# Optimization experiments

Measured on AMD Instinct MI355X. Metric: run time of the kernel, lower is better.

The kernel has to match this reference:

```python
import jax, jax.numpy as jnp
import numpy as np

WS = 6          # window size
NUM_HEADS = 6
HEAD_DIM = 32   # dim=192 / 6 heads
SCALE = HEAD_DIM ** -0.5


def _rel_pos_index(ws):
    # Faithful to the torch buffer construction (torch.meshgrid default 'ij').
    coords = np.stack(np.meshgrid(np.arange(ws), np.arange(ws), np.arange(ws), indexing='ij'))  # [3,ws,ws,ws]
    flat = coords.reshape(3, -1)                       # [3, ws^3]
    rel = flat[:, :, None] - flat[:, None, :]          # [3, N, N]
    rel = rel.transpose(1, 2, 0).astype(np.int64)      # [N, N, 3]
    rel += ws - 1
    rel[..., 0] *= 3 * ws - 1
    rel[..., 1] *= 2 * ws - 1
    return rel.sum(-1)                                 # [N, N]

REL_INDEX = jnp.asarray(_rel_pos_index(WS))            # [216, 216] int


def setup_inputs() -> dict:
    key = jax.random.key(0)
    k1, k2, k3, k4 = jax.random.split(key, 4)
    B, N, C = 1024, WS ** 3, NUM_HEADS * HEAD_DIM
    return {
        "x": jax.random.normal(k1, (B, N, C), dtype=jnp.float32),
        "qkv_w": jax.random.normal(k2, (3 * C, C), dtype=jnp.float32) * 0.02,
        "proj_w": jax.random.normal(k3, (C, C), dtype=jnp.float32) * 0.02,
        "proj_b": jnp.zeros((C,), dtype=jnp.float32),
        "bias_table": jax.random.normal(k4, ((2 * WS - 1) ** 3, NUM_HEADS), dtype=jnp.float32) * 0.02,
    }


def reference(x, qkv_w, proj_w, proj_b, bias_table):
    B, N, C = x.shape
    H, D = NUM_HEADS, HEAD_DIM
    qkv = jnp.einsum('bnc,fc->bnf', x, qkv_w)              # [B,N,3C]
    qkv = qkv.reshape(B, N, 3, H, D).transpose(2, 0, 3, 1, 4)  # [3,B,H,N,D]
    q, k, v = qkv[0], qkv[1], qkv[2]
    attn = jnp.einsum('bhnd,bhmd->bhnm', q * SCALE, k)     # [B,H,N,N]
    bias = bias_table[REL_INDEX]                           # [N,N,H]
    attn = attn + bias.transpose(2, 0, 1)[None]            # add [1,H,N,N]
    attn = jax.nn.softmax(attn, axis=-1)
    out = jnp.einsum('bhnm,bhmd->bhnd', attn, v)           # [B,H,N,D]
    out = out.transpose(0, 2, 1, 3).reshape(B, N, C)
    return jnp.einsum('bnc,oc->bno', out, proj_w) + proj_b
```

## Files before the change

kernel.cpp:

```cpp
#include <hip/hip_runtime.h>
#include <cstdint>
#include <cstddef>


typedef __attribute__((ext_vector_type(8))) short short8;
typedef __attribute__((ext_vector_type(4))) float f32x4;
typedef unsigned short u16;
typedef unsigned int   u32;

#define SCALE_F 0.17677669529663687f

#define QS_OFF   0
#define KS_OFF   17920
#define VT_OFF   35840
#define PCH_OFF  50688
#define ATTN_LDS 68608

#define PROJ_LDS 76800

__device__ __forceinline__ u16 f2bf(float f) {
  union { float f; u32 u; } v; v.f = f;
  return (u16)((v.u + 0x7fffu + ((v.u >> 16) & 1u)) >> 16);
}

__device__ __forceinline__ f32x4 mfma16(short8 a, short8 b, f32x4 c) {
  return __builtin_amdgcn_mfma_f32_16x16x32_bf16(a, b, c, 0, 0, 0);
}

__global__ void prep_kernel(const float* __restrict__ x,
                            const float* __restrict__ qkv_w,
                            const float* __restrict__ proj_w,
                            const float* __restrict__ bias_table,
                            u16* __restrict__ wb,
                            u16* __restrict__ pwb,
                            u16* __restrict__ biasp,
                            float* outbuf) {
  const int tid = blockIdx.x * blockDim.x + threadIdx.x;
  const int stride = gridDim.x * blockDim.x;
  const float4* x4 = (const float4*)x;
  for (int i = tid; i < 1024 * 10368; i += stride) {
    const int b = i / 10368, r = i % 10368;
    const float4 v = x4[i];
    union { u16 s[4]; unsigned long long u; } pk;
    pk.s[0] = f2bf(v.x); pk.s[1] = f2bf(v.y);
    pk.s[2] = f2bf(v.z); pk.s[3] = f2bf(v.w);
    *(unsigned long long*)((u16*)(outbuf + (size_t)b * 41472) + 41472 + r * 4) = pk.u;
  }
  for (int i = tid; i < 576 * 192; i += stride) wb[i] = f2bf(qkv_w[i]);
  for (int i = tid; i < 192 * 192; i += stride) pwb[i] = f2bf(proj_w[i]);
  for (int i = tid; i < 6 * 7 * 16 * 224 * 2; i += stride) {
    const int t = i & 1;
    int j = i >> 1;
    const int n = j % 224; j /= 224;
    const int l = j & 15;  j >>= 4;
    const int c = j % 7;
    const int h = j / 7;
    const int m = c * 32 + t * 16 + l;
    u16 val;
    if (n >= 216)      val = 0;
    else if (m >= 216) val = 0xFF80;
    else {
      const int di = n / 36 - m / 36;
      const int dj = (n / 6) % 6 - (m / 6) % 6;
      const int dk = n % 6 - m % 6;
      const int idx = (di + 5) * 17 + (dj + 5) * 11 + (dk + 5);
      val = f2bf(bias_table[idx * 6 + h]);
    }
    biasp[i] = val;
  }
}

__global__ __launch_bounds__(1024, 8)
void attn_kernel(const u16* __restrict__ wb, const u16* __restrict__ biasp,
                 float* outbuf) {
  extern __shared__ char smem[];
  u16* qs  = (u16*)(smem + QS_OFF);
  u16* ks  = (u16*)(smem + KS_OFF);
  u16* vT  = (u16*)(smem + VT_OFF);
  u16* pch = (u16*)(smem + PCH_OFF);

  const int b = blockIdx.x;
  const int tid = threadIdx.x;
  const int wave = tid >> 6;
  const int lane = tid & 63;
  const int quad = lane >> 4;
  const int lcol = lane & 15;

  const u16* xb   = (const u16*)(outbuf + (size_t)b * 41472) + 41472;
  u16*       attnb = (u16*)(outbuf + (size_t)b * 41472);

  for (int i = tid; i < 8 * 40; i += 1024) { qs[216 * 40 + i] = 0; ks[216 * 40 + i] = 0; }
  for (int i = tid; i < 32 * 8; i += 1024) {
    const int d = i >> 3, jj = i & 7;
    vT[d * 232 + 209 + 2 * jj] = 0;
  }
  __syncthreads();

  for (int h = 0; h < 6; ++h) {
    for (int u = wave; u < 14; u += 16) {
      f32x4 acc[6] = {};
      const int ar0 = u * 16 + lcol;
      const int ar  = ar0 < 216 ? ar0 : 215;
#pragma unroll
      for (int kk = 0; kk < 6; ++kk) {
        const short8 a = *(const short8*)(xb + ar * 192 + kk * 32 + quad * 8);
#pragma unroll
        for (int j = 0; j < 6; ++j) {
          const int fbase = (j >> 1) * 192 + h * 32 + (j & 1) * 16;
          const short8 bf = *(const short8*)(wb + (fbase + lcol) * 192 + kk * 32 + quad * 8);
          acc[j] = mfma16(a, bf, acc[j]);
        }
      }
      const int nb = u * 16 + quad * 4;
#pragma unroll
      for (int r = 0; r < 4; ++r) {
        const int n = nb + r;
        if (n < 216) {
          *(u32*)(qs + n * 40 + 2 * lcol) =
              (u32)f2bf(acc[0][r]) | ((u32)f2bf(acc[1][r]) << 16);
          *(u32*)(ks + n * 40 + 2 * lcol) =
              (u32)f2bf(acc[2][r]) | ((u32)f2bf(acc[3][r]) << 16);
          const int pm = (n & ~31) | (2 * (n & 15)) | ((n >> 4) & 1);
          vT[lcol * 232 + pm]        = f2bf(acc[4][r]);
          vT[(16 + lcol) * 232 + pm] = f2bf(acc[5][r]);
        }
      }
    }
    __syncthreads();

    if (wave < 14) {
      const int s = wave;
      u16* pw_ = pch + wave * 640;

      uint4 bias_q[7];
#pragma unroll
      for (int c = 0; c < 7; ++c)
        bias_q[c] = *(const uint4*)(biasp + ((size_t)((h * 7 + c) * 16 + lcol)) * 448
                                    + (s * 16 + quad * 4) * 2);
      const short8 qa = *(const short8*)(qs + (s * 16 + lcol) * 40 + quad * 8);

      u32 pP[7][4];
      f32x4 rsum = {};
#pragma unroll
      for (int c = 0; c < 7; ++c) {
        const short8 kb0 = *(const short8*)(ks + (c * 32 + lcol) * 40 + quad * 8);
        const short8 kb1 = *(const short8*)(ks + (c * 32 + 16 + lcol) * 40 + quad * 8);
        const f32x4 z = {};
        const f32x4 s0 = mfma16(qa, kb0, z);
        const f32x4 s1 = mfma16(qa, kb1, z);
        const u32* bw = (const u32*)&bias_q[c];
#pragma unroll
        for (int r = 0; r < 4; ++r) {
          union { u32 u; float f; } b0, b1;
          b0.u = bw[r] << 16;
          b1.u = bw[r] & 0xFFFF0000u;
          const float p0 = __expf(__builtin_fmaf(s0[r], SCALE_F, b0.f));
          const float p1 = __expf(__builtin_fmaf(s1[r], SCALE_F, b1.f));
          rsum[r] += p0 + p1;
          pP[c][r] = (u32)f2bf(p0) | ((u32)f2bf(p1) << 16);
        }
      }

      f32x4 o0 = {}, o1 = {};
#pragma unroll
      for (int c = 0; c < 7; ++c) {
#pragma unroll
        for (int r = 0; r < 4; ++r)
          *(u32*)(pw_ + (quad * 4 + r) * 40 + 2 * lcol) = pP[c][r];
        __builtin_amdgcn_s_waitcnt(0);
        const short8 pa  = *(const short8*)(pw_ + lcol * 40 + quad * 8);
        const short8 vb0 = *(const short8*)(vT + lcol * 232 + c * 32 + quad * 8);
        const short8 vb1 = *(const short8*)(vT + (16 + lcol) * 232 + c * 32 + quad * 8);
        o0 = mfma16(pa, vb0, o0);
        o1 = mfma16(pa, vb1, o1);
      }

      f32x4 inv;
#pragma unroll
      for (int r = 0; r < 4; ++r) {
        float ssum = rsum[r];
        ssum += __shfl_xor(ssum, 1, 16);
        ssum += __shfl_xor(ssum, 2, 16);
        ssum += __shfl_xor(ssum, 4, 16);
        ssum += __shfl_xor(ssum, 8, 16);
        inv[r] = 1.0f / ssum;
      }
#pragma unroll
      for (int r = 0; r < 4; ++r) {
        const int n = s * 16 + quad * 4 + r;
        if (n < 216) {
          attnb[n * 192 + h * 32 + lcol]      = f2bf(o0[r] * inv[r]);
          attnb[n * 192 + h * 32 + 16 + lcol] = f2bf(o1[r] * inv[r]);
        }
      }
    }
    __syncthreads();
  }
}

__global__ __launch_bounds__(1024, 8)
void proj_kernel(const u16* __restrict__ pwb, const float* __restrict__ proj_b,
                 float* outbuf) {
  extern __shared__ char smem[];
  u16* pws = (u16*)smem;
  const int b = blockIdx.x, tid = threadIdx.x;
  const int wave = tid >> 6, lane = tid & 63, quad = lane >> 4, lcol = lane & 15;
  float* myout = outbuf + (size_t)b * 41472;
  const u16* attnb = (const u16*)myout;

  for (int i = tid; i < 192 * 24; i += 1024) {
    const int row = i / 24, c8 = i % 24;
    *(short8*)(pws + row * 200 + c8 * 8) = *(const short8*)(pwb + row * 192 + c8 * 8);
  }

  short8 a[6] = {};
  const bool active = wave < 14;
  if (active) {
    const int arow = wave * 16 + lcol;
    if (arow < 216) {
#pragma unroll
      for (int kk = 0; kk < 6; ++kk)
        a[kk] = *(const short8*)(attnb + arow * 192 + kk * 32 + quad * 8);
    }
  }
  __syncthreads();

  if (active) {
    for (int nt = 0; nt < 12; ++nt) {
      f32x4 acc = {};
#pragma unroll
      for (int kk = 0; kk < 6; ++kk) {
        const short8 bf = *(const short8*)(pws + (nt * 16 + lcol) * 200 + kk * 32 + quad * 8);
        acc = mfma16(a[kk], bf, acc);
      }
      const float pbv = proj_b[nt * 16 + lcol];
      const int nb = wave * 16 + quad * 4;
#pragma unroll
      for (int r = 0; r < 4; ++r) {
        const int n = nb + r;
        if (n < 216) myout[n * 192 + nt * 16 + lcol] = acc[r] + pbv;
      }
    }
  }
}

extern "C" void kernel_launch(void* const* d_in, const int* in_sizes, int n_in,
                              void* d_out, int out_size, void* d_ws, size_t ws_size,
                              hipStream_t stream) {
  (void)in_sizes; (void)n_in; (void)out_size; (void)ws_size;
  const float* x          = (const float*)d_in[0];
  const float* qkv_w      = (const float*)d_in[1];
  const float* proj_w     = (const float*)d_in[2];
  const float* proj_b     = (const float*)d_in[3];
  const float* bias_table = (const float*)d_in[4];
  float* out = (float*)d_out;

  u16* wb    = (u16*)d_ws;
  u16* pwb   = (u16*)((char*)d_ws + 221184);
  u16* biasp = (u16*)((char*)d_ws + 294912);

  (void)hipFuncSetAttribute((const void*)attn_kernel,
                            hipFuncAttributeMaxDynamicSharedMemorySize, ATTN_LDS);
  (void)hipFuncSetAttribute((const void*)proj_kernel,
                            hipFuncAttributeMaxDynamicSharedMemorySize, PROJ_LDS);

  prep_kernel<<<dim3(1024), dim3(256), 0, stream>>>(x, qkv_w, proj_w, bias_table,
                                                    wb, pwb, biasp, out);
  attn_kernel<<<dim3(1024), dim3(1024), ATTN_LDS, stream>>>(wb, biasp, out);
  proj_kernel<<<dim3(1024), dim3(1024), PROJ_LDS, stream>>>(pwb, proj_b, out);
}
```

Baseline: 812.7 us.

## Compute transposed scores so P feeds PV MFMA from registers, drop LDS staging

The score MFMA is computed as K·Qᵀ, so each lane holds a column of P in the layout the PV MFMA A-operand expects. This removes the per-chunk LDS round trip with s_waitcnt for P, and removes that LDS region. To match, V's column permutation and the bias table layout are rearranged, and the softmax row sum is now reduced across quads. The shuffled inverse is then broadcast back per row. Blocks shrink from 1024 to 896 threads so all 14 waves do work and no idle waves remain, at the cost of more complex index permutations that must stay consistent.

```diff
diff --git a/kernel.cpp b/kernel.cpp
--- a/kernel.cpp
+++ b/kernel.cpp
@@ -13,8 +13,7 @@
 #define QS_OFF   0
 #define KS_OFF   17920
 #define VT_OFF   35840
-#define PCH_OFF  50688
-#define ATTN_LDS 68608
+#define ATTN_LDS 50688
 
 #define PROJ_LDS 76800
 
@@ -48,11 +47,11 @@
   }
   for (int i = tid; i < 576 * 192; i += stride) wb[i] = f2bf(qkv_w[i]);
   for (int i = tid; i < 192 * 192; i += stride) pwb[i] = f2bf(proj_w[i]);
-  for (int i = tid; i < 6 * 7 * 16 * 224 * 2; i += stride) {
+  for (int i = tid; i < 6 * 7 * 224 * 16 * 2; i += stride) {
     const int t = i & 1;
     int j = i >> 1;
+    const int l = j & 15;  j >>= 4;
     const int n = j % 224; j /= 224;
-    const int l = j & 15;  j >>= 4;
     const int c = j % 7;
     const int h = j / 7;
     const int m = c * 32 + t * 16 + l;
@@ -70,14 +69,13 @@
   }
 }
 
-__global__ __launch_bounds__(1024, 8)
+__global__ __launch_bounds__(896, 7)
 void attn_kernel(const u16* __restrict__ wb, const u16* __restrict__ biasp,
                  float* outbuf) {
   extern __shared__ char smem[];
   u16* qs  = (u16*)(smem + QS_OFF);
   u16* ks  = (u16*)(smem + KS_OFF);
   u16* vT  = (u16*)(smem + VT_OFF);
-  u16* pch = (u16*)(smem + PCH_OFF);
 
   const int b = blockIdx.x;
   const int tid = threadIdx.x;
@@ -86,18 +84,19 @@
   const int quad = lane >> 4;
   const int lcol = lane & 15;
 
-  const u16* xb   = (const u16*)(outbuf + (size_t)b * 41472) + 41472;
+  const u16* xb    = (const u16*)(outbuf + (size_t)b * 41472) + 41472;
   u16*       attnb = (u16*)(outbuf + (size_t)b * 41472);
 
-  for (int i = tid; i < 8 * 40; i += 1024) { qs[216 * 40 + i] = 0; ks[216 * 40 + i] = 0; }
-  for (int i = tid; i < 32 * 8; i += 1024) {
+  for (int i = tid; i < 8 * 40; i += 896) { qs[216 * 40 + i] = 0; ks[216 * 40 + i] = 0; }
+  for (int i = tid; i < 32 * 8; i += 896) {
     const int d = i >> 3, jj = i & 7;
-    vT[d * 232 + 209 + 2 * jj] = 0;
+    vT[d * 232 + 192 + 20 + (jj & 3) + ((jj >> 2) << 3)] = 0;
   }
   __syncthreads();
 
   for (int h = 0; h < 6; ++h) {
-    for (int u = wave; u < 14; u += 16) {
+    {
+      const int u = wave;
       f32x4 acc[6] = {};
       const int ar0 = u * 16 + lcol;
       const int ar  = ar0 < 216 ? ar0 : 215;
@@ -120,7 +119,7 @@
               (u32)f2bf(acc[0][r]) | ((u32)f2bf(acc[1][r]) << 16);
           *(u32*)(ks + n * 40 + 2 * lcol) =
               (u32)f2bf(acc[2][r]) | ((u32)f2bf(acc[3][r]) << 16);
-          const int pm = (n & ~31) | (2 * (n & 15)) | ((n >> 4) & 1);
+          const int pm = (n & ~31) | (((n >> 2) & 3) << 3) | (((n >> 4) & 1) << 2) | (n & 3);
           vT[lcol * 232 + pm]        = f2bf(acc[4][r]);
           vT[(16 + lcol) * 232 + pm] = f2bf(acc[5][r]);
         }
@@ -128,69 +127,51 @@
     }
     __syncthreads();
 
-    if (wave < 14) {
+    {
       const int s = wave;
-      u16* pw_ = pch + wave * 640;
-
-      uint4 bias_q[7];
-#pragma unroll
-      for (int c = 0; c < 7; ++c)
-        bias_q[c] = *(const uint4*)(biasp + ((size_t)((h * 7 + c) * 16 + lcol)) * 448
-                                    + (s * 16 + quad * 4) * 2);
       const short8 qa = *(const short8*)(qs + (s * 16 + lcol) * 40 + quad * 8);
-
-      u32 pP[7][4];
-      f32x4 rsum = {};
+      f32x4 o0 = {}, o1 = {};
+      float rsum = 0.0f;
 #pragma unroll
       for (int c = 0; c < 7; ++c) {
         const short8 kb0 = *(const short8*)(ks + (c * 32 + lcol) * 40 + quad * 8);
         const short8 kb1 = *(const short8*)(ks + (c * 32 + 16 + lcol) * 40 + quad * 8);
         const f32x4 z = {};
-        const f32x4 s0 = mfma16(qa, kb0, z);
-        const f32x4 s1 = mfma16(qa, kb1, z);
-        const u32* bw = (const u32*)&bias_q[c];
+        const f32x4 s0 = mfma16(kb0, qa, z);
+        const f32x4 s1 = mfma16(kb1, qa, z);
+        const uint4 bq = *(const uint4*)(biasp
+            + ((size_t)((h * 7 + c) * 224 + s * 16 + lcol)) * 32 + quad * 8);
+        const u32* bw = (const u32*)&bq;
+        float p0[4], p1[4];
 #pragma unroll
         for (int r = 0; r < 4; ++r) {
           union { u32 u; float f; } b0, b1;
           b0.u = bw[r] << 16;
           b1.u = bw[r] & 0xFFFF0000u;
-          const float p0 = __expf(__builtin_fmaf(s0[r], SCALE_F, b0.f));
-          const float p1 = __expf(__builtin_fmaf(s1[r], SCALE_F, b1.f));
-          rsum[r] += p0 + p1;
-          pP[c][r] = (u32)f2bf(p0) | ((u32)f2bf(p1) << 16);
-        }
-      }
-
-      f32x4 o0 = {}, o1 = {};
-#pragma unroll
-      for (int c = 0; c < 7; ++c) {
-#pragma unroll
-        for (int r = 0; r < 4; ++r)
-          *(u32*)(pw_ + (quad * 4 + r) * 40 + 2 * lcol) = pP[c][r];
-        __builtin_amdgcn_s_waitcnt(0);
-        const short8 pa  = *(const short8*)(pw_ + lcol * 40 + quad * 8);
+          p0[r] = __expf(__builtin_fmaf(s0[r], SCALE_F, b0.f));
+          p1[r] = __expf(__builtin_fmaf(s1[r], SCALE_F, b1.f));
+          rsum += p0[r] + p1[r];
+        }
+        union { u32 w[4]; short8 v; } pk;
+        pk.w[0] = (u32)f2bf(p0[0]) | ((u32)f2bf(p0[1]) << 16);
+        pk.w[1] = (u32)f2bf(p0[2]) | ((u32)f2bf(p0[3]) << 16);
+        pk.w[2] = (u32)f2bf(p1[0]) | ((u32)f2bf(p1[1]) << 16);
+        pk.w[3] = (u32)f2bf(p1[2]) | ((u32)f2bf(p1[3]) << 16);
         const short8 vb0 = *(const short8*)(vT + lcol * 232 + c * 32 + quad * 8);
         const short8 vb1 = *(const short8*)(vT + (16 + lcol) * 232 + c * 32 + quad * 8);
-        o0 = mfma16(pa, vb0, o0);
-        o1 = mfma16(pa, vb1, o1);
-      }
-
-      f32x4 inv;
+        o0 = mfma16(pk.v, vb0, o0);
+        o1 = mfma16(pk.v, vb1, o1);
+      }
+      rsum += __shfl_xor(rsum, 16);
+      rsum += __shfl_xor(rsum, 32);
+      const float inv = 1.0f / rsum;
 #pragma unroll
       for (int r = 0; r < 4; ++r) {
-        float ssum = rsum[r];
-        ssum += __shfl_xor(ssum, 1, 16);
-        ssum += __shfl_xor(ssum, 2, 16);
-        ssum += __shfl_xor(ssum, 4, 16);
-        ssum += __shfl_xor(ssum, 8, 16);
-        inv[r] = 1.0f / ssum;
-      }
-#pragma unroll
-      for (int r = 0; r < 4; ++r) {
+        const float invr = __shfl(inv, quad * 4 + r, 16);
         const int n = s * 16 + quad * 4 + r;
         if (n < 216) {
-          attnb[n * 192 + h * 32 + lcol]      = f2bf(o0[r] * inv[r]);
-          attnb[n * 192 + h * 32 + 16 + lcol] = f2bf(o1[r] * inv[r]);
+          attnb[n * 192 + h * 32 + lcol]      = f2bf(o0[r] * invr);
+          attnb[n * 192 + h * 32 + 16 + lcol] = f2bf(o1[r] * invr);
         }
       }
     }
@@ -198,7 +179,7 @@
   }
 }
 
-__global__ __launch_bounds__(1024, 8)
+__global__ __launch_bounds__(896, 7)
 void proj_kernel(const u16* __restrict__ pwb, const float* __restrict__ proj_b,
                  float* outbuf) {
   extern __shared__ char smem[];
@@ -208,14 +189,13 @@
   float* myout = outbuf + (size_t)b * 41472;
   const u16* attnb = (const u16*)myout;
 
-  for (int i = tid; i < 192 * 24; i += 1024) {
+  for (int i = tid; i < 192 * 24; i += 896) {
     const int row = i / 24, c8 = i % 24;
     *(short8*)(pws + row * 200 + c8 * 8) = *(const short8*)(pwb + row * 192 + c8 * 8);
   }
 
   short8 a[6] = {};
-  const bool active = wave < 14;
-  if (active) {
+  {
     const int arow = wave * 16 + lcol;
     if (arow < 216) {
 #pragma unroll
@@ -225,21 +205,19 @@
   }
   __syncthreads();
 
-  if (active) {
-    for (int nt = 0; nt < 12; ++nt) {
-      f32x4 acc = {};
-#pragma unroll
-      for (int kk = 0; kk < 6; ++kk) {
-        const short8 bf = *(const short8*)(pws + (nt * 16 + lcol) * 200 + kk * 32 + quad * 8);
-        acc = mfma16(a[kk], bf, acc);
-      }
-      const float pbv = proj_b[nt * 16 + lcol];
-      const int nb = wave * 16 + quad * 4;
-#pragma unroll
-      for (int r = 0; r < 4; ++r) {
-        const int n = nb + r;
-        if (n < 216) myout[n * 192 + nt * 16 + lcol] = acc[r] + pbv;
-      }
+  for (int nt = 0; nt < 12; ++nt) {
+    f32x4 acc = {};
+#pragma unroll
+    for (int kk = 0; kk < 6; ++kk) {
+      const short8 bf = *(const short8*)(pws + (nt * 16 + lcol) * 200 + kk * 32 + quad * 8);
+      acc = mfma16(a[kk], bf, acc);
+    }
+    const float pbv = proj_b[nt * 16 + lcol];
+    const int nb = wave * 16 + quad * 4;
+#pragma unroll
+    for (int r = 0; r < 4; ++r) {
+      const int n = nb + r;
+      if (n < 216) myout[n * 192 + nt * 16 + lcol] = acc[r] + pbv;
     }
   }
 }
@@ -266,6 +244,6 @@
 
   prep_kernel<<<dim3(1024), dim3(256), 0, stream>>>(x, qkv_w, proj_w, bias_table,
                                                     wb, pwb, biasp, out);
-  attn_kernel<<<dim3(1024), dim3(1024), ATTN_LDS, stream>>>(wb, biasp, out);
-  proj_kernel<<<dim3(1024), dim3(1024), PROJ_LDS, stream>>>(pwb, proj_b, out);
-}
+  attn_kernel<<<dim3(1024), dim3(896), ATTN_LDS, stream>>>(wb, biasp, out);
+  proj_kernel<<<dim3(1024), dim3(896), PROJ_LDS, stream>>>(pwb, proj_b, out);
+}
```

Result: slower. 876.9 us (+7.9%).
